# Kernel optimization log

Hardware: AMD Instinct MI355X
Metric: run time of the kernel (lower is better)

## Reference

```python
import jax, jax.numpy as jnp
import numpy as np

N, E, F_IN, HID, HEADS, NCLS, NG = 50000, 800000, 128, 128, 4, 10, 512
C = HID // HEADS          # per-head channels
BN_EPS = 1e-5
NEG_SLOPE = 0.2           # SuperGATConv default negative_slope
N_CONV = 3


def setup_inputs() -> dict:
    key = jax.random.key(0)
    ks = jax.random.split(key, 16)
    x = jax.random.normal(ks[0], (N, F_IN), jnp.float32)
    # edges with no self loops (reference appends self loops itself, as SuperGATConv does)
    src = jax.random.randint(ks[1], (E,), 0, N, dtype=jnp.int32)
    off = jax.random.randint(ks[2], (E,), 1, N, dtype=jnp.int32)
    dst = (src + off) % N
    edge_index = jnp.stack([src, dst], axis=0)
    batch = jnp.sort(jax.random.randint(ks[3], (N,), 0, NG, dtype=jnp.int32))
    s = 0.1
    # BatchNorm params per module init: weight=1, bias=1e-4 (running stats fresh: mean=0, var=1)
    inp = {
        "x": x, "edge_index": edge_index, "batch": batch,
        "bn_feat_g": jnp.ones((F_IN,), jnp.float32), "bn_feat_b": jnp.full((F_IN,), 1e-4, jnp.float32),
        "w_feat": jax.random.normal(ks[4], (F_IN, HID), jnp.float32) * s,
        "b_feat": jnp.zeros((HID,), jnp.float32),
        "bn_conv_g": jnp.ones((N_CONV, HID), jnp.float32), "bn_conv_b": jnp.full((N_CONV, HID), 1e-4, jnp.float32),
        "w_gat": jax.random.normal(ks[5], (N_CONV, HID, HID), jnp.float32) * s,
        "att_l": jax.random.normal(ks[6], (N_CONV, HEADS, C), jnp.float32) * s,
        "att_r": jax.random.normal(ks[7], (N_CONV, HEADS, C), jnp.float32) * s,
        "b_gat": jnp.zeros((N_CONV, HID), jnp.float32),
        "bn_fc_g": jnp.ones((HID,), jnp.float32), "bn_fc_b": jnp.full((HID,), 1e-4, jnp.float32),
        "w_fc": jax.random.normal(ks[8], (HID, HID), jnp.float32) * s,
        "b_fc": jnp.zeros((HID,), jnp.float32),
        "bn_hid_g": jnp.ones((HID,), jnp.float32), "bn_hid_b": jnp.full((HID,), 1e-4, jnp.float32),
        "w_cls": jax.random.normal(ks[9], (HID, NCLS), jnp.float32) * s,
        "b_cls": jnp.zeros((NCLS,), jnp.float32),
    }
    return inp


def _bn_eval(h, g, b):
    # eval-mode BatchNorm1d with fresh running stats (mean=0, var=1)
    return h * (g / jnp.sqrt(1.0 + BN_EPS)) + b


def _segment_softmax(a, seg, num_segments):
    # softmax over edges grouped by destination node (PyG softmax semantics)
    m = jax.ops.segment_max(a, seg, num_segments=num_segments)
    a = jnp.exp(a - m[seg])
    s = jax.ops.segment_sum(a, seg, num_segments=num_segments)
    return a / (s[seg] + 1e-16)


def _supergat_mx(h, src, dst, W, att_l, att_r, bias):
    # h: [N, HID] -> per-head features [N, H, C]
    hh = (h @ W).reshape(N, HEADS, C)
    h_j = hh[src]  # source (message) features  [E2, H, C]
    h_i = hh[dst]  # destination features       [E2, H, C]
    logits = jnp.einsum('ehc,ehc->eh', h_i, h_j)                       # MX dot-product
    alpha = jnp.einsum('ehc,hc->eh', h_j, att_l) + jnp.einsum('ehc,hc->eh', h_i, att_r)
    alpha = alpha * jax.nn.sigmoid(logits)
    alpha = jax.nn.leaky_relu(alpha, NEG_SLOPE)
    alpha = _segment_softmax(alpha, dst, N)                            # [E2, H]
    out = jax.ops.segment_sum(h_j * alpha[..., None], dst, num_segments=N)
    return out.reshape(N, HID) + bias


def reference(x, edge_index, batch, bn_feat_g, bn_feat_b, w_feat, b_feat,
              bn_conv_g, bn_conv_b, w_gat, att_l, att_r, b_gat,
              bn_fc_g, bn_fc_b, w_fc, b_fc, bn_hid_g, bn_hid_b, w_cls, b_cls):
    loops = jnp.arange(N, dtype=edge_index.dtype)
    src = jnp.concatenate([edge_index[0], loops])   # SuperGATConv adds self loops
    dst = jnp.concatenate([edge_index[1], loops])
    h = _bn_eval(x, bn_feat_g, bn_feat_b)
    h = jax.nn.relu(h @ w_feat + b_feat)            # GCNConv(gfn=True) == Linear
    for i in range(N_CONV):
        h = _bn_eval(h, bn_conv_g[i], bn_conv_b[i])
        h = jax.nn.relu(_supergat_mx(h, src, dst, w_gat[i], att_l[i], att_r[i], b_gat[i]))
    g = jax.ops.segment_sum(h, batch, num_segments=NG)  # global_add_pool -> [NG, HID]
    g = _bn_eval(g, bn_fc_g, bn_fc_b)
    g = jax.nn.relu(g @ w_fc + b_fc)
    g = _bn_eval(g, bn_hid_g, bn_hid_b)
    logits = g @ w_cls + b_cls
    att_loss = jnp.float32(0.0)  # eval mode: no edge-sampled attention loss
    return jax.nn.log_softmax(logits, axis=-1), att_loss
```

## Files before the change

### kernel.cpp

```cpp
#include <hip/hip_runtime.h>

#define NN 50000
#define EE 800000
#define FHID 128
#define NHEAD 4
#define NGRAPH 512
#define NCLS 10
#define BK 256
#define BCH 4096
#define NBLK_E 196
#define NBUCK 196
#define CAPB 6144

typedef unsigned short u16;
typedef unsigned int u32;
typedef unsigned long long u64;
typedef __attribute__((ext_vector_type(8))) short bf16x8;
typedef __attribute__((ext_vector_type(4))) float f32x4;

__device__ __forceinline__ float bf2f(u16 u){
    union { u32 i; float f; } v; v.i = ((u32)u) << 16; return v.f;
}
__device__ __forceinline__ float bflo(u32 u){
    union { u32 i; float f; } v; v.i = u << 16; return v.f;
}
__device__ __forceinline__ float bfhi(u32 u){
    union { u32 i; float f; } v; v.i = u & 0xffff0000u; return v.f;
}
__device__ __forceinline__ u16 f2bf(float f){
    union { float f; u32 i; } v; v.f = f;
    u32 r = v.i + 0x7fffu + ((v.i >> 16) & 1u);
    return (u16)(r >> 16);
}
__device__ __forceinline__ u32 pack2(float a, float b){
    return ((u32)f2bf(b) << 16) | f2bf(a);
}
__device__ __forceinline__ float loadF(const void* p, int i, int isf32){
    return isf32 ? ((const float*)p)[i] : bf2f(((const u16*)p)[i]);
}
__device__ __forceinline__ void unpk8(uint4 v, float* f){
    f[0]=bflo(v.x); f[1]=bfhi(v.x);
    f[2]=bflo(v.y); f[3]=bfhi(v.y);
    f[4]=bflo(v.z); f[5]=bfhi(v.z);
    f[6]=bflo(v.w); f[7]=bfhi(v.w);
}

__device__ int detect_local(const u16* x, int tid, int nthreads, int* lds){
    int ok = 0;
    for (int i = tid; i < 1024; i += nthreads){
        u16 u = x[i];
        int e = (u >> 7) & 0xFF;
        if ((u & 0x7fff) == 0 || (e >= 0x70 && e <= 0x85)) ok++;
    }
    lds[tid] = ok;
    __syncthreads();
    for (int o2 = nthreads >> 1; o2 > 0; o2 >>= 1){
        if (tid < o2) lds[tid] += lds[tid + o2];
        __syncthreads();
    }
    int r = (lds[0] < 900) ? 1 : 0;
    __syncthreads();
    return r;
}

__global__ __launch_bounds__(256) void prep_all(
        const u16* __restrict__ xz,
        const void* w_feat, const void* b_feat, const void* bn_feat_g, const void* bn_feat_b,
        const void* w_gat, const void* bn_conv_g, const void* bn_conv_b, const void* b_gat,
        const void* wfc, const void* bfc, const void* bnfg, const void* bnfb,
        const void* bnhg, const void* bnhb, const void* wcls, const void* bcls,
        const void* attl, const void* attr,
        u16* __restrict__ Wt, float* __restrict__ cvec, float* __restrict__ biasv,
        float* __restrict__ hp, int* __restrict__ dflag, int* __restrict__ gcur)
{
    __shared__ int ldsi[256];
    __shared__ float red[128];
    int bid = blockIdx.x, t = threadIdx.x;
    int isf32 = detect_local(xz, t, 256, ldsi);
    if (bid == 0){
        if (t == 0) dflag[0] = isf32;
        gcur[t] = t * CAPB;
    }

    if (bid < 512){
        if (t >= 128) return;
        int L = bid >> 7;
        int n = bid & 127;
        int k = t;
        const float rs = rsqrtf(1.0f + 1e-5f);
        float wv, bg, bb;
        if (L == 0){
            wv = loadF(w_feat, k*FHID + n, isf32);
            bg = loadF(bn_feat_g, k, isf32);
            bb = loadF(bn_feat_b, k, isf32);
        } else {
            wv = loadF(w_gat, (L-1)*FHID*FHID + k*FHID + n, isf32);
            bg = loadF(bn_conv_g, (L-1)*FHID + k, isf32);
            bb = loadF(bn_conv_b, (L-1)*FHID + k, isf32);
        }
        Wt[L*FHID*FHID + n*FHID + k] = f2bf(bg * rs * wv);
        red[k] = bb * wv;
        __syncthreads();
        for (int o2 = 64; o2 > 0; o2 >>= 1){
            if (k < o2) red[k] += red[k + o2];
            __syncthreads();
        }
        if (k == 0){
            float c = red[0];
            if (L == 0) c += loadF(b_feat, n, isf32);
            cvec[L*FHID + n] = c;
            if (L > 0) biasv[L*FHID + n] = loadF(b_gat, (L-1)*FHID + n, isf32);
        }
    } else {
        int gt = (bid - 512)*256 + t;
        for (int i = gt; i < FHID*FHID; i += 16*256) hp[i] = loadF(wfc, i, isf32);
        if (gt < FHID*NCLS) hp[16384 + gt] = loadF(wcls, gt, isf32);
        if (gt >= 2048 && gt < 2048 + 3*FHID){
            int i = gt - 2048;
            hp[18320 + i] = loadF(attl, i, isf32);
            hp[18704 + i] = loadF(attr, i, isf32);
        }
        if (gt >= 2560 && gt < 2560 + FHID){
            int tt = gt - 2560;
            hp[17664 + tt] = loadF(bnfg, tt, isf32);
            hp[17792 + tt] = loadF(bnfb, tt, isf32);
            hp[17920 + tt] = loadF(bfc,  tt, isf32);
            hp[18048 + tt] = loadF(bnhg, tt, isf32);
            hp[18176 + tt] = loadF(bnhb, tt, isf32);
        }
        if (gt >= 3072 && gt < 3072 + NCLS) hp[18304 + (gt - 3072)] = loadF(bcls, gt - 3072, isf32);
    }
}

__global__ __launch_bounds__(256) void gemm128(const void* __restrict__ A,
                                               const u16* __restrict__ Wt,
                                               const float* __restrict__ cvec,
                                               u16* __restrict__ out, int relu,
                                               int araw, const int* __restrict__ flag,
                                               const float* __restrict__ attl,
                                               const float* __restrict__ attr,
                                               float* __restrict__ al,
                                               float* __restrict__ ar)
{
    int wave = threadIdx.x >> 6;
    int lane = threadIdx.x & 63;
    int m = lane & 15, quad = lane >> 4;
    int rowbase = blockIdx.x * 128 + wave * 32;
    bool f32in = araw && flag[0];
    const u16*  Au = (const u16*)A;
    const float* Af = (const float*)A;
    int r0 = rowbase + m, r1 = rowbase + 16 + m;
    bool v0 = r0 < NN, v1 = r1 < NN;
    f32x4 acc[2][8];
#pragma unroll
    for (int i = 0; i < 2; i++)
#pragma unroll
        for (int j = 0; j < 8; j++) acc[i][j] = (f32x4){0.f,0.f,0.f,0.f};
#pragma unroll
    for (int t = 0; t < 4; t++){
        bf16x8 a0 = {0,0,0,0,0,0,0,0}, a1 = {0,0,0,0,0,0,0,0};
        int kof = t*32 + quad*8;
        if (f32in){
            if (v0){
                const float* p = Af + (size_t)r0*FHID + kof;
                float4 u0 = *(const float4*)p, u1 = *(const float4*)(p+4);
                a0[0]=(short)f2bf(u0.x); a0[1]=(short)f2bf(u0.y);
                a0[2]=(short)f2bf(u0.z); a0[3]=(short)f2bf(u0.w);
                a0[4]=(short)f2bf(u1.x); a0[5]=(short)f2bf(u1.y);
                a0[6]=(short)f2bf(u1.z); a0[7]=(short)f2bf(u1.w);
            }
            if (v1){
                const float* p = Af + (size_t)r1*FHID + kof;
                float4 u0 = *(const float4*)p, u1 = *(const float4*)(p+4);
                a1[0]=(short)f2bf(u0.x); a1[1]=(short)f2bf(u0.y);
                a1[2]=(short)f2bf(u0.z); a1[3]=(short)f2bf(u0.w);
                a1[4]=(short)f2bf(u1.x); a1[5]=(short)f2bf(u1.y);
                a1[6]=(short)f2bf(u1.z); a1[7]=(short)f2bf(u1.w);
            }
        } else {
            if (v0) a0 = *(const bf16x8*)(Au + (size_t)r0*FHID + kof);
            if (v1) a1 = *(const bf16x8*)(Au + (size_t)r1*FHID + kof);
        }
#pragma unroll
        for (int ct = 0; ct < 8; ct++){
            bf16x8 wfrag = *(const bf16x8*)(Wt + (ct*16 + m)*FHID + kof);
            acc[0][ct] = __builtin_amdgcn_mfma_f32_16x16x32_bf16(wfrag, a0, acc[0][ct], 0, 0, 0);
            acc[1][ct] = __builtin_amdgcn_mfma_f32_16x16x32_bf16(wfrag, a1, acc[1][ct], 0, 0, 0);
        }
    }
    bool doa = (attl != nullptr);
#pragma unroll
    for (int tt = 0; tt < 2; tt++){
        int row = rowbase + tt*16 + m;
        bool rv = row < NN;
        float sl[4] = {0.f,0.f,0.f,0.f};
        float sr[4] = {0.f,0.f,0.f,0.f};
#pragma unroll
        for (int ct = 0; ct < 8; ct++){
            int cb = ct*16 + quad*4;
            float4 cv = *(const float4*)(cvec + cb);
            float w0 = acc[tt][ct][0] + cv.x;
            float w1 = acc[tt][ct][1] + cv.y;
            float w2 = acc[tt][ct][2] + cv.z;
            float w3 = acc[tt][ct][3] + cv.w;
            if (relu){
                w0 = fmaxf(w0, 0.f); w1 = fmaxf(w1, 0.f);
                w2 = fmaxf(w2, 0.f); w3 = fmaxf(w3, 0.f);
            }
            if (doa){
                int h = ct >> 1;
                float4 tl = *(const float4*)(attl + cb);
                float4 tr = *(const float4*)(attr + cb);
                sl[h] += w0*tl.x + w1*tl.y + w2*tl.z + w3*tl.w;
                sr[h] += w0*tr.x + w1*tr.y + w2*tr.z + w3*tr.w;
            }
            if (rv){
                uint2 st; st.x = pack2(w0, w1); st.y = pack2(w2, w3);
                *(uint2*)(out + (size_t)row*FHID + cb) = st;
            }
        }
        if (doa){
#pragma unroll
            for (int h = 0; h < 4; h++){
                sl[h] += __shfl_xor(sl[h], 16, 64);
                sl[h] += __shfl_xor(sl[h], 32, 64);
                sr[h] += __shfl_xor(sr[h], 16, 64);
                sr[h] += __shfl_xor(sr[h], 32, 64);
            }
            if (rv){
                al[row*NHEAD + quad] = sl[quad];
                ar[row*NHEAD + quad] = sr[quad];
            }
        }
    }
}

__global__ __launch_bounds__(256) void bin_edges(const int* __restrict__ srcp,
        const int* __restrict__ dstp, int* __restrict__ gcur, u64* __restrict__ binned)
{
    __shared__ int h[BK], lb[BK], gb[BK], cur[BK];
    __shared__ u64 stage[BCH];
    int t = threadIdx.x;
    h[t] = 0;
    __syncthreads();
    int base = blockIdx.x * BCH;
    int sv[16], dv[16];
#pragma unroll
    for (int k = 0; k < 16; k++){
        int e = base + k*256 + t;
        int d = -1, s = 0;
        if (e < EE){
            d = dstp[e]; s = srcp[e];
            if ((u32)d >= NN) d = -1;
        }
        sv[k] = s; dv[k] = d;
        if (d >= 0) atomicAdd(&h[d >> 8], 1);
    }
    __syncthreads();
    lb[t] = h[t];
    __syncthreads();
    for (int off = 1; off < BK; off <<= 1){
        int x = (t >= off) ? lb[t - off] : 0;
        __syncthreads();
        lb[t] += x;
        __syncthreads();
    }
    int excl = lb[t] - h[t];
    int tot  = lb[BK-1];
    __syncthreads();
    lb[t] = excl;
    gb[t] = h[t] ? atomicAdd(&gcur[t], h[t]) : 0;
    cur[t] = 0;
    __syncthreads();
#pragma unroll
    for (int k = 0; k < 16; k++){
        int d = dv[k];
        if (d >= 0){
            int b = d >> 8;
            int p = lb[b] + atomicAdd(&cur[b], 1);
            stage[p] = ((u64)(u32)d << 32) | (u32)sv[k];
        }
    }
    __syncthreads();
    for (int i = t; i < tot; i += 256){
        u64 pr = stage[i];
        int b = (int)(pr >> 40);
        binned[gb[b] + (i - lb[b])] = pr;
    }
}

__global__ __launch_bounds__(256) void build_csr(const u64* __restrict__ binned,
        const int* __restrict__ gcur, int2* __restrict__ rowdeg, int* __restrict__ colbuf)
{
    __shared__ int deg[BK], ls[BK], cur[BK];
    __shared__ int colstage[CAPB];
    int b = blockIdx.x, t = threadIdx.x;
    int gb = b * CAPB;
    int cnt = gcur[b] - gb;
    if (cnt < 0) cnt = 0;
    if (cnt > CAPB) cnt = CAPB;
    deg[t] = 0;
    __syncthreads();
    for (int i = t; i < cnt; i += 256){
        int d = (int)(binned[gb + i] >> 32);
        atomicAdd(&deg[d & 255], 1);
    }
    __syncthreads();
    ls[t] = deg[t];
    __syncthreads();
    for (int off = 1; off < BK; off <<= 1){
        int x = (t >= off) ? ls[t - off] : 0;
        __syncthreads();
        ls[t] += x;
        __syncthreads();
    }
    int excl = ls[t] - deg[t];
    int node = b*256 + t;
    if (node < NN) rowdeg[node] = (int2){gb + excl, gb + excl + deg[t]};
    cur[t] = excl;
    __syncthreads();
    for (int i = t; i < cnt; i += 256){
        u64 pr = binned[gb + i];
        int d = (int)(pr >> 32) & 255;
        int s = (int)(u32)pr;
        int p = atomicAdd(&cur[d], 1);
        colstage[p] = s;
    }
    __syncthreads();
    for (int i = t; i < cnt; i += 256) colbuf[gb + i] = colstage[i];
}

__global__ __launch_bounds__(256) void supergat_conv(const u16* __restrict__ hh,
        const float* __restrict__ al, const float* __restrict__ ar,
        const int2* __restrict__ rowdeg, const int* __restrict__ colbuf,
        const float* __restrict__ bias, u16* __restrict__ hout)
{
    int wid  = (blockIdx.x*256 + threadIdx.x) >> 6;
    int lane = threadIdx.x & 63;
    int group = lane >> 4;
    int gl    = lane & 15;
    int head  = gl >> 2;
    int q     = gl & 3;
    int node  = wid*4 + group;
    bool valid = node < NN;
    int snode = valid ? node : 0;
    int chbase = head*32 + q*8;

    uint4 hdv = *(const uint4*)(hh + (size_t)snode*FHID + chbase);
    float hd[8]; unpk8(hdv, hd);
    float arn = ar[snode*NHEAD + head];
    float aln = al[snode*NHEAD + head];

    float d = hd[0]*hd[0]+hd[1]*hd[1]+hd[2]*hd[2]+hd[3]*hd[3]
            + hd[4]*hd[4]+hd[5]*hd[5]+hd[6]*hd[6]+hd[7]*hd[7];
    d += __shfl_xor(d, 1, 64);
    d += __shfl_xor(d, 2, 64);
    float a = (aln + arn) * (1.0f / (1.0f + __expf(-d)));
    a = (a > 0.0f) ? a : 0.2f*a;
    float p = __expf(fminf(a, 60.f));
    float s = p;
    float o[8];
#pragma unroll
    for (int i = 0; i < 8; i++) o[i] = p*hd[i];

    int2 rd = valid ? rowdeg[node] : (int2){0,0};
    int e0 = rd.x, e1 = rd.y;
    if (e0 < 0) e0 = 0;
    if (e1 > BK*CAPB) e1 = BK*CAPB;

    int e = e0;
    while (e + 3 < e1){
        int sidx[4]; uint4 xv[4]; float af[4];
#pragma unroll
        for (int j = 0; j < 4; j++){
            int si = colbuf[e + j];
            if ((u32)si >= NN) si = 0;
            sidx[j] = si;
        }
#pragma unroll
        for (int j = 0; j < 4; j++){
            xv[j] = *(const uint4*)(hh + (size_t)sidx[j]*FHID + chbase);
            af[j] = al[sidx[j]*NHEAD + head];
        }
#pragma unroll
        for (int j = 0; j < 4; j++){
            float hs[8]; unpk8(xv[j], hs);
            float lg = hd[0]*hs[0]+hd[1]*hs[1]+hd[2]*hs[2]+hd[3]*hs[3]
                     + hd[4]*hs[4]+hd[5]*hs[5]+hd[6]*hs[6]+hd[7]*hs[7];
            lg += __shfl_xor(lg, 1, 64);
            lg += __shfl_xor(lg, 2, 64);
            float a2 = (af[j] + arn) * (1.0f / (1.0f + __expf(-lg)));
            a2 = (a2 > 0.0f) ? a2 : 0.2f*a2;
            float pe = __expf(fminf(a2, 60.f));
            s += pe;
#pragma unroll
            for (int i = 0; i < 8; i++) o[i] += pe*hs[i];
        }
        e += 4;
    }
    while (e < e1){
        int si = colbuf[e];
        if ((u32)si >= NN) si = 0;
        uint4 x1 = *(const uint4*)(hh + (size_t)si*FHID + chbase);
        float af1 = al[si*NHEAD + head];
        float hs[8]; unpk8(x1, hs);
        float lg = hd[0]*hs[0]+hd[1]*hs[1]+hd[2]*hs[2]+hd[3]*hs[3]
                 + hd[4]*hs[4]+hd[5]*hs[5]+hd[6]*hs[6]+hd[7]*hs[7];
        lg += __shfl_xor(lg, 1, 64);
        lg += __shfl_xor(lg, 2, 64);
        float a2 = (af1 + arn) * (1.0f / (1.0f + __expf(-lg)));
        a2 = (a2 > 0.0f) ? a2 : 0.2f*a2;
        float pe = __expf(fminf(a2, 60.f));
        s += pe;
#pragma unroll
        for (int i = 0; i < 8; i++) o[i] += pe*hs[i];
        e++;
    }

    if (valid){
        float inv = 1.0f / (s + 1e-16f);
        uint4 w;
        w.x = pack2(fmaxf(o[0]*inv + bias[chbase+0], 0.f),
                    fmaxf(o[1]*inv + bias[chbase+1], 0.f));
        w.y = pack2(fmaxf(o[2]*inv + bias[chbase+2], 0.f),
                    fmaxf(o[3]*inv + bias[chbase+3], 0.f));
        w.z = pack2(fmaxf(o[4]*inv + bias[chbase+4], 0.f),
                    fmaxf(o[5]*inv + bias[chbase+5], 0.f));
        w.w = pack2(fmaxf(o[6]*inv + bias[chbase+6], 0.f),
                    fmaxf(o[7]*inv + bias[chbase+7], 0.f));
        *(uint4*)(hout + (size_t)node*FHID + chbase) = w;
    }
}

__global__ void pool_head(const u16* __restrict__ h, const int* __restrict__ batch,
                          const float* __restrict__ hp, const int* __restrict__ flag,
                          void* __restrict__ out)
{
    __shared__ int bounds[2];
    __shared__ float gb[FHID];
    __shared__ float g2[FHID];
    __shared__ float lg[16];
    int gi = blockIdx.x, t = threadIdx.x;
    int isf32 = flag[0];
    if (t < 2){
        int target = gi + t;
        int lo = 0, hi = NN;
        while (lo < hi){
            int mid = (lo + hi) >> 1;
            if (batch[mid] < target) lo = mid + 1; else hi = mid;
        }
        bounds[t] = lo;
    }
    __syncthreads();
    float acc0 = 0.f;
    for (int node = bounds[0]; node < bounds[1]; node++)
        acc0 += bf2f(h[(size_t)node*FHID + t]);
    const float rs = rsqrtf(1.0f + 1e-5f);
    gb[t] = acc0 * (hp[17664 + t] * rs) + hp[17792 + t];
    __syncthreads();
    float acc = hp[17920 + t];
    for (int k = 0; k < FHID; k++) acc += gb[k] * hp[k*FHID + t];
    acc = fmaxf(acc, 0.f);
    g2[t] = acc * (hp[18048 + t] * rs) + hp[18176 + t];
    __syncthreads();
    if (t < NCLS){
        float l = hp[18304 + t];
        for (int k = 0; k < FHID; k++) l += g2[k] * hp[16384 + k*NCLS + t];
        lg[t] = l;
    }
    __syncthreads();
    if (t == 0){
        float mx = lg[0];
        for (int j = 1; j < NCLS; j++) mx = fmaxf(mx, lg[j]);
        float se = 0.f;
        for (int j = 0; j < NCLS; j++) se += __expf(lg[j] - mx);
        float lse = logf(se) + mx;
        if (isf32){
            float* o = (float*)out;
            for (int j = 0; j < NCLS; j++) o[gi*NCLS + j] = lg[j] - lse;
            if (gi == 0) o[NGRAPH*NCLS] = 0.f;
        } else {
            u16* o = (u16*)out;
            for (int j = 0; j < NCLS; j++) o[gi*NCLS + j] = f2bf(lg[j] - lse);
            if (gi == 0) o[NGRAPH*NCLS] = 0;
        }
    }
}

extern "C" void kernel_launch(void* const* d_in, const int* in_sizes, int n_in,
                              void* d_out, int out_size, void* d_ws, size_t ws_size,
                              hipStream_t stream)
{
    (void)in_sizes; (void)n_in; (void)out_size; (void)ws_size;
    const void* x         = d_in[0];
    const int* edge       = (const int*)d_in[1];
    const int* batch      = (const int*)d_in[2];

    char* ws = (char*)d_ws;
    size_t off = 0;
    auto alloc = [&](size_t bytes) -> char* {
        char* p = ws + off; off += (bytes + 255) & ~(size_t)255; return p;
    };
    int*   dflag   = (int*)  alloc(256);
    u16*   WtAll   = (u16*)  alloc((size_t)4*FHID*FHID*2);
    float* cvecAll = (float*)alloc((size_t)4*FHID*4);
    float* biasv   = (float*)alloc((size_t)4*FHID*4);
    float* headp   = (float*)alloc((size_t)19088*4);
    float* al      = (float*)alloc((size_t)NN*NHEAD*4);
    float* ar      = (float*)alloc((size_t)NN*NHEAD*4);
    int*   gcur    = (int*)  alloc((size_t)BK*4);
    int2*  rowdeg  = (int2*) alloc((size_t)NN*8);
    int*   colbuf  = (int*)  alloc((size_t)BK*CAPB*4);
    u16*   hA      = (u16*)  alloc((size_t)NN*FHID*2);
    u16*   hB      = (u16*)  alloc((size_t)NN*FHID*2);
    u64*   binned  = (u64*)hB;

    const int* srcp = edge;
    const int* dstp = edge + EE;

    prep_all<<<528, 256, 0, stream>>>((const u16*)x,
        d_in[5], d_in[6], d_in[3], d_in[4], d_in[9], d_in[7], d_in[8], d_in[12],
        d_in[15], d_in[16], d_in[13], d_in[14], d_in[17], d_in[18], d_in[19], d_in[20],
        d_in[10], d_in[11],
        WtAll, cvecAll, biasv, headp, dflag, gcur);

    bin_edges<<<NBLK_E, 256, 0, stream>>>(srcp, dstp, gcur, binned);
    build_csr<<<NBUCK, 256, 0, stream>>>(binned, gcur, rowdeg, colbuf);

    gemm128<<<(NN + 127)/128, 256, 0, stream>>>(x, WtAll, cvecAll, hA, 1, 1, dflag,
                                                nullptr, nullptr, nullptr, nullptr);

    for (int i = 0; i < 3; i++){
        gemm128<<<(NN + 127)/128, 256, 0, stream>>>(hA, WtAll + (i+1)*FHID*FHID,
                                                    cvecAll + (i+1)*FHID, hB, 0, 0, dflag,
                                                    headp + 18320 + i*FHID,
                                                    headp + 18704 + i*FHID, al, ar);
        supergat_conv<<<(NN + 15)/16, 256, 0, stream>>>(hB, al, ar, rowdeg, colbuf,
                                                        biasv + (i+1)*FHID, hA);
    }

    pool_head<<<NGRAPH, 128, 0, stream>>>(hA, batch, headp, dflag, d_out);
}
```

Before: 389.7 us.

## Software-pipeline edge gathers, use DPP reductions, retile GEMM and edge binning

The supergat_conv edge loop becomes double-buffered: the next group of four neighbor rows and attention logits is loaded while the current group is computed. A masked tail replaces the scalar remainder loop, and colbuf is padded so the over-read stays in bounds. Quad reductions switch from shuffles to DPP moves. The GEMM drops to 16 rows per wave to double the grid, bin_edges uses smaller chunks across more blocks, build_csr runs with 512 threads, and pool_head unrolls its node sum into four accumulators. These changes target latency-bound gathers and low occupancy, at the cost of more weight-fragment reloads per row in the GEMM and more atomics in binning.

```diff
diff --git a/kernel.cpp b/kernel.cpp
--- a/kernel.cpp
+++ b/kernel.cpp
@@ -7,8 +7,8 @@
 #define NGRAPH 512
 #define NCLS 10
 #define BK 256
-#define BCH 4096
-#define NBLK_E 196
+#define BCH 2048
+#define NBLK_E 391
 #define NBUCK 196
 #define CAPB 6144
 
@@ -43,6 +43,13 @@
     f[2]=bflo(v.y); f[3]=bfhi(v.y);
     f[4]=bflo(v.z); f[5]=bfhi(v.z);
     f[6]=bflo(v.w); f[7]=bfhi(v.w);
+}
+
+__device__ __forceinline__ float quad_red(float x){
+    int t0 = __builtin_amdgcn_mov_dpp(__float_as_int(x), 0xB1, 0xF, 0xF, true);
+    float y = x + __int_as_float(t0);
+    int t1 = __builtin_amdgcn_mov_dpp(__float_as_int(y), 0x4E, 0xF, 0xF, true);
+    return y + __int_as_float(t1);
 }
 
 __device__ int detect_local(const u16* x, int tid, int nthreads, int* lds){
@@ -145,92 +152,74 @@
     int wave = threadIdx.x >> 6;
     int lane = threadIdx.x & 63;
     int m = lane & 15, quad = lane >> 4;
-    int rowbase = blockIdx.x * 128 + wave * 32;
+    int row = blockIdx.x * 64 + wave * 16 + m;
+    bool v0 = row < NN;
     bool f32in = araw && flag[0];
     const u16*  Au = (const u16*)A;
     const float* Af = (const float*)A;
-    int r0 = rowbase + m, r1 = rowbase + 16 + m;
-    bool v0 = r0 < NN, v1 = r1 < NN;
-    f32x4 acc[2][8];
-#pragma unroll
-    for (int i = 0; i < 2; i++)
-#pragma unroll
-        for (int j = 0; j < 8; j++) acc[i][j] = (f32x4){0.f,0.f,0.f,0.f};
+    f32x4 acc[8];
+#pragma unroll
+    for (int j = 0; j < 8; j++) acc[j] = (f32x4){0.f,0.f,0.f,0.f};
 #pragma unroll
     for (int t = 0; t < 4; t++){
-        bf16x8 a0 = {0,0,0,0,0,0,0,0}, a1 = {0,0,0,0,0,0,0,0};
+        bf16x8 a0 = {0,0,0,0,0,0,0,0};
         int kof = t*32 + quad*8;
         if (f32in){
             if (v0){
-                const float* p = Af + (size_t)r0*FHID + kof;
+                const float* p = Af + (size_t)row*FHID + kof;
                 float4 u0 = *(const float4*)p, u1 = *(const float4*)(p+4);
                 a0[0]=(short)f2bf(u0.x); a0[1]=(short)f2bf(u0.y);
                 a0[2]=(short)f2bf(u0.z); a0[3]=(short)f2bf(u0.w);
                 a0[4]=(short)f2bf(u1.x); a0[5]=(short)f2bf(u1.y);
                 a0[6]=(short)f2bf(u1.z); a0[7]=(short)f2bf(u1.w);
             }
-            if (v1){
-                const float* p = Af + (size_t)r1*FHID + kof;
-                float4 u0 = *(const float4*)p, u1 = *(const float4*)(p+4);
-                a1[0]=(short)f2bf(u0.x); a1[1]=(short)f2bf(u0.y);
-                a1[2]=(short)f2bf(u0.z); a1[3]=(short)f2bf(u0.w);
-                a1[4]=(short)f2bf(u1.x); a1[5]=(short)f2bf(u1.y);
-                a1[6]=(short)f2bf(u1.z); a1[7]=(short)f2bf(u1.w);
-            }
         } else {
-            if (v0) a0 = *(const bf16x8*)(Au + (size_t)r0*FHID + kof);
-            if (v1) a1 = *(const bf16x8*)(Au + (size_t)r1*FHID + kof);
+            if (v0) a0 = *(const bf16x8*)(Au + (size_t)row*FHID + kof);
         }
 #pragma unroll
         for (int ct = 0; ct < 8; ct++){
             bf16x8 wfrag = *(const bf16x8*)(Wt + (ct*16 + m)*FHID + kof);
-            acc[0][ct] = __builtin_amdgcn_mfma_f32_16x16x32_bf16(wfrag, a0, acc[0][ct], 0, 0, 0);
-            acc[1][ct] = __builtin_amdgcn_mfma_f32_16x16x32_bf16(wfrag, a1, acc[1][ct], 0, 0, 0);
+            acc[ct] = __builtin_amdgcn_mfma_f32_16x16x32_bf16(wfrag, a0, acc[ct], 0, 0, 0);
         }
     }
     bool doa = (attl != nullptr);
-#pragma unroll
-    for (int tt = 0; tt < 2; tt++){
-        int row = rowbase + tt*16 + m;
-        bool rv = row < NN;
-        float sl[4] = {0.f,0.f,0.f,0.f};
-        float sr[4] = {0.f,0.f,0.f,0.f};
-#pragma unroll
-        for (int ct = 0; ct < 8; ct++){
-            int cb = ct*16 + quad*4;
-            float4 cv = *(const float4*)(cvec + cb);
-            float w0 = acc[tt][ct][0] + cv.x;
-            float w1 = acc[tt][ct][1] + cv.y;
-            float w2 = acc[tt][ct][2] + cv.z;
-            float w3 = acc[tt][ct][3] + cv.w;
-            if (relu){
-                w0 = fmaxf(w0, 0.f); w1 = fmaxf(w1, 0.f);
-                w2 = fmaxf(w2, 0.f); w3 = fmaxf(w3, 0.f);
-            }
-            if (doa){
-                int h = ct >> 1;
-                float4 tl = *(const float4*)(attl + cb);
-                float4 tr = *(const float4*)(attr + cb);
-                sl[h] += w0*tl.x + w1*tl.y + w2*tl.z + w3*tl.w;
-                sr[h] += w0*tr.x + w1*tr.y + w2*tr.z + w3*tr.w;
-            }
-            if (rv){
-                uint2 st; st.x = pack2(w0, w1); st.y = pack2(w2, w3);
-                *(uint2*)(out + (size_t)row*FHID + cb) = st;
-            }
+    float sl[4] = {0.f,0.f,0.f,0.f};
+    float sr[4] = {0.f,0.f,0.f,0.f};
+#pragma unroll
+    for (int ct = 0; ct < 8; ct++){
+        int cb = ct*16 + quad*4;
+        float4 cv = *(const float4*)(cvec + cb);
+        float w0 = acc[ct][0] + cv.x;
+        float w1 = acc[ct][1] + cv.y;
+        float w2 = acc[ct][2] + cv.z;
+        float w3 = acc[ct][3] + cv.w;
+        if (relu){
+            w0 = fmaxf(w0, 0.f); w1 = fmaxf(w1, 0.f);
+            w2 = fmaxf(w2, 0.f); w3 = fmaxf(w3, 0.f);
         }
         if (doa){
-#pragma unroll
-            for (int h = 0; h < 4; h++){
-                sl[h] += __shfl_xor(sl[h], 16, 64);
-                sl[h] += __shfl_xor(sl[h], 32, 64);
-                sr[h] += __shfl_xor(sr[h], 16, 64);
-                sr[h] += __shfl_xor(sr[h], 32, 64);
-            }
-            if (rv){
-                al[row*NHEAD + quad] = sl[quad];
-                ar[row*NHEAD + quad] = sr[quad];
-            }
+            int h = ct >> 1;
+            float4 tl = *(const float4*)(attl + cb);
+            float4 tr = *(const float4*)(attr + cb);
+            sl[h] += w0*tl.x + w1*tl.y + w2*tl.z + w3*tl.w;
+            sr[h] += w0*tr.x + w1*tr.y + w2*tr.z + w3*tr.w;
+        }
+        if (v0){
+            uint2 st; st.x = pack2(w0, w1); st.y = pack2(w2, w3);
+            *(uint2*)(out + (size_t)row*FHID + cb) = st;
+        }
+    }
+    if (doa){
+#pragma unroll
+        for (int h = 0; h < 4; h++){
+            sl[h] += __shfl_xor(sl[h], 16, 64);
+            sl[h] += __shfl_xor(sl[h], 32, 64);
+            sr[h] += __shfl_xor(sr[h], 16, 64);
+            sr[h] += __shfl_xor(sr[h], 32, 64);
+        }
+        if (v0){
+            al[row*NHEAD + quad] = sl[quad];
+            ar[row*NHEAD + quad] = sr[quad];
         }
     }
 }
@@ -244,9 +233,9 @@
     h[t] = 0;
     __syncthreads();
     int base = blockIdx.x * BCH;
-    int sv[16], dv[16];
-#pragma unroll
-    for (int k = 0; k < 16; k++){
+    int sv[8], dv[8];
+#pragma unroll
+    for (int k = 0; k < 8; k++){
         int e = base + k*256 + t;
         int d = -1, s = 0;
         if (e < EE){
@@ -273,7 +262,7 @@
     cur[t] = 0;
     __syncthreads();
 #pragma unroll
-    for (int k = 0; k < 16; k++){
+    for (int k = 0; k < 8; k++){
         int d = dv[k];
         if (d >= 0){
             int b = d >> 8;
@@ -289,7 +278,7 @@
     }
 }
 
-__global__ __launch_bounds__(256) void build_csr(const u64* __restrict__ binned,
+__global__ __launch_bounds__(512) void build_csr(const u64* __restrict__ binned,
         const int* __restrict__ gcur, int2* __restrict__ rowdeg, int* __restrict__ colbuf)
 {
     __shared__ int deg[BK], ls[BK], cur[BK];
@@ -299,27 +288,29 @@
     int cnt = gcur[b] - gb;
     if (cnt < 0) cnt = 0;
     if (cnt > CAPB) cnt = CAPB;
-    deg[t] = 0;
-    __syncthreads();
-    for (int i = t; i < cnt; i += 256){
+    if (t < BK) deg[t] = 0;
+    __syncthreads();
+    for (int i = t; i < cnt; i += 512){
         int d = (int)(binned[gb + i] >> 32);
         atomicAdd(&deg[d & 255], 1);
     }
     __syncthreads();
-    ls[t] = deg[t];
+    if (t < BK) ls[t] = deg[t];
     __syncthreads();
     for (int off = 1; off < BK; off <<= 1){
-        int x = (t >= off) ? ls[t - off] : 0;
+        int x = (t < BK && t >= off) ? ls[t - off] : 0;
         __syncthreads();
-        ls[t] += x;
+        if (t < BK) ls[t] += x;
         __syncthreads();
     }
-    int excl = ls[t] - deg[t];
-    int node = b*256 + t;
-    if (node < NN) rowdeg[node] = (int2){gb + excl, gb + excl + deg[t]};
-    cur[t] = excl;
-    __syncthreads();
-    for (int i = t; i < cnt; i += 256){
+    if (t < BK){
+        int excl = ls[t] - deg[t];
+        int node = b*256 + t;
+        if (node < NN) rowdeg[node] = (int2){gb + excl, gb + excl + deg[t]};
+        cur[t] = excl;
+    }
+    __syncthreads();
+    for (int i = t; i < cnt; i += 512){
         u64 pr = binned[gb + i];
         int d = (int)(pr >> 32) & 255;
         int s = (int)(u32)pr;
@@ -327,7 +318,56 @@
         colstage[p] = s;
     }
     __syncthreads();
-    for (int i = t; i < cnt; i += 256) colbuf[gb + i] = colstage[i];
+    for (int i = t; i < cnt; i += 512) colbuf[gb + i] = colstage[i];
+}
+
+struct EdgeGrp {
+    uint4 x0, x1, x2, x3;
+    float f0, f1, f2, f3;
+};
+
+__device__ __forceinline__ void load_grp(EdgeGrp& G, const int* __restrict__ colbuf,
+        int g, const u16* __restrict__ hh, const float* __restrict__ al,
+        int chbase, int head)
+{
+    int i0 = colbuf[g+0], i1 = colbuf[g+1], i2 = colbuf[g+2], i3 = colbuf[g+3];
+    if ((u32)i0 >= NN) i0 = 0;
+    if ((u32)i1 >= NN) i1 = 0;
+    if ((u32)i2 >= NN) i2 = 0;
+    if ((u32)i3 >= NN) i3 = 0;
+    G.x0 = *(const uint4*)(hh + (size_t)i0*FHID + chbase);
+    G.x1 = *(const uint4*)(hh + (size_t)i1*FHID + chbase);
+    G.x2 = *(const uint4*)(hh + (size_t)i2*FHID + chbase);
+    G.x3 = *(const uint4*)(hh + (size_t)i3*FHID + chbase);
+    G.f0 = al[i0*NHEAD + head];
+    G.f1 = al[i1*NHEAD + head];
+    G.f2 = al[i2*NHEAD + head];
+    G.f3 = al[i3*NHEAD + head];
+}
+
+__device__ __forceinline__ void comp_edge(uint4 xv, float af, bool ev,
+        const float* hd, float arn, float& s, float* o)
+{
+    float hs[8]; unpk8(xv, hs);
+    float lg = hd[0]*hs[0]+hd[1]*hs[1]+hd[2]*hs[2]+hd[3]*hs[3]
+             + hd[4]*hs[4]+hd[5]*hs[5]+hd[6]*hs[6]+hd[7]*hs[7];
+    lg = quad_red(lg);
+    float a2 = (af + arn) * (1.0f / (1.0f + __expf(-lg)));
+    a2 = (a2 > 0.0f) ? a2 : 0.2f*a2;
+    float pe = __expf(fminf(a2, 60.f));
+    if (!ev) pe = 0.f;
+    s += pe;
+#pragma unroll
+    for (int i = 0; i < 8; i++) o[i] += pe*hs[i];
+}
+
+__device__ __forceinline__ void comp_grp(const EdgeGrp& G, int g, int e1,
+        const float* hd, float arn, float& s, float* o)
+{
+    comp_edge(G.x0, G.f0, g+0 < e1, hd, arn, s, o);
+    comp_edge(G.x1, G.f1, g+1 < e1, hd, arn, s, o);
+    comp_edge(G.x2, G.f2, g+2 < e1, hd, arn, s, o);
+    comp_edge(G.x3, G.f3, g+3 < e1, hd, arn, s, o);
 }
 
 __global__ __launch_bounds__(256) void supergat_conv(const u16* __restrict__ hh,
@@ -353,8 +393,7 @@
 
     float d = hd[0]*hd[0]+hd[1]*hd[1]+hd[2]*hd[2]+hd[3]*hd[3]
             + hd[4]*hd[4]+hd[5]*hd[5]+hd[6]*hd[6]+hd[7]*hd[7];
-    d += __shfl_xor(d, 1, 64);
-    d += __shfl_xor(d, 2, 64);
+    d = quad_red(d);
     float a = (aln + arn) * (1.0f / (1.0f + __expf(-d)));
     a = (a > 0.0f) ? a : 0.2f*a;
     float p = __expf(fminf(a, 60.f));
@@ -368,53 +407,21 @@
     if (e0 < 0) e0 = 0;
     if (e1 > BK*CAPB) e1 = BK*CAPB;
 
-    int e = e0;
-    while (e + 3 < e1){
-        int sidx[4]; uint4 xv[4]; float af[4];
-#pragma unroll
-        for (int j = 0; j < 4; j++){
-            int si = colbuf[e + j];
-            if ((u32)si >= NN) si = 0;
-            sidx[j] = si;
-        }
-#pragma unroll
-        for (int j = 0; j < 4; j++){
-            xv[j] = *(const uint4*)(hh + (size_t)sidx[j]*FHID + chbase);
-            af[j] = al[sidx[j]*NHEAD + head];
-        }
-#pragma unroll
-        for (int j = 0; j < 4; j++){
-            float hs[8]; unpk8(xv[j], hs);
-            float lg = hd[0]*hs[0]+hd[1]*hs[1]+hd[2]*hs[2]+hd[3]*hs[3]
-                     + hd[4]*hs[4]+hd[5]*hs[5]+hd[6]*hs[6]+hd[7]*hs[7];
-            lg += __shfl_xor(lg, 1, 64);
-            lg += __shfl_xor(lg, 2, 64);
-            float a2 = (af[j] + arn) * (1.0f / (1.0f + __expf(-lg)));
-            a2 = (a2 > 0.0f) ? a2 : 0.2f*a2;
-            float pe = __expf(fminf(a2, 60.f));
-            s += pe;
-#pragma unroll
-            for (int i = 0; i < 8; i++) o[i] += pe*hs[i];
-        }
-        e += 4;
-    }
-    while (e < e1){
-        int si = colbuf[e];
-        if ((u32)si >= NN) si = 0;
-        uint4 x1 = *(const uint4*)(hh + (size_t)si*FHID + chbase);
-        float af1 = al[si*NHEAD + head];
-        float hs[8]; unpk8(x1, hs);
-        float lg = hd[0]*hs[0]+hd[1]*hs[1]+hd[2]*hs[2]+hd[3]*hs[3]
-                 + hd[4]*hs[4]+hd[5]*hs[5]+hd[6]*hs[6]+hd[7]*hs[7];
-        lg += __shfl_xor(lg, 1, 64);
-        lg += __shfl_xor(lg, 2, 64);
-        float a2 = (af1 + arn) * (1.0f / (1.0f + __expf(-lg)));
-        a2 = (a2 > 0.0f) ? a2 : 0.2f*a2;
-        float pe = __expf(fminf(a2, 60.f));
-        s += pe;
-#pragma unroll
-        for (int i = 0; i < 8; i++) o[i] += pe*hs[i];
-        e++;
+    EdgeGrp A, B;
+    int g = e0;
+    if (g < e1){
+        load_grp(A, colbuf, g, hh, al, chbase, head);
+        while (true){
+            int gn = g + 4;
+            if (gn >= e1){ comp_grp(A, g, e1, hd, arn, s, o); break; }
+            load_grp(B, colbuf, gn, hh, al, chbase, head);
+            comp_grp(A, g, e1, hd, arn, s, o);
+            g = gn; gn = g + 4;
+            if (gn >= e1){ comp_grp(B, g, e1, hd, arn, s, o); break; }
+            load_grp(A, colbuf, gn, hh, al, chbase, head);
+            comp_grp(B, g, e1, hd, arn, s, o);
+            g = gn;
+        }
     }
 
     if (valid){
@@ -452,9 +459,16 @@
         bounds[t] = lo;
     }
     __syncthreads();
-    float acc0 = 0.f;
-    for (int node = bounds[0]; node < bounds[1]; node++)
-        acc0 += bf2f(h[(size_t)node*FHID + t]);
+    float s0 = 0.f, s1 = 0.f, s2 = 0.f, s3 = 0.f;
+    int node = bounds[0], nend = bounds[1];
+    for (; node + 3 < nend; node += 4){
+        s0 += bf2f(h[(size_t)(node+0)*FHID + t]);
+        s1 += bf2f(h[(size_t)(node+1)*FHID + t]);
+        s2 += bf2f(h[(size_t)(node+2)*FHID + t]);
+        s3 += bf2f(h[(size_t)(node+3)*FHID + t]);
+    }
+    for (; node < nend; node++) s0 += bf2f(h[(size_t)node*FHID + t]);
+    float acc0 = (s0 + s1) + (s2 + s3);
     const float rs = rsqrtf(1.0f + 1e-5f);
     gb[t] = acc0 * (hp[17664 + t] * rs) + hp[17792 + t];
     __syncthreads();
@@ -510,7 +524,7 @@
     float* ar      = (float*)alloc((size_t)NN*NHEAD*4);
     int*   gcur    = (int*)  alloc((size_t)BK*4);
     int2*  rowdeg  = (int2*) alloc((size_t)NN*8);
-    int*   colbuf  = (int*)  alloc((size_t)BK*CAPB*4);
+    int*   colbuf  = (int*)  alloc((size_t)(BK*CAPB + 16)*4);
     u16*   hA      = (u16*)  alloc((size_t)NN*FHID*2);
     u16*   hB      = (u16*)  alloc((size_t)NN*FHID*2);
     u64*   binned  = (u64*)hB;
@@ -525,16 +539,16 @@
         WtAll, cvecAll, biasv, headp, dflag, gcur);
 
     bin_edges<<<NBLK_E, 256, 0, stream>>>(srcp, dstp, gcur, binned);
-    build_csr<<<NBUCK, 256, 0, stream>>>(binned, gcur, rowdeg, colbuf);
-
-    gemm128<<<(NN + 127)/128, 256, 0, stream>>>(x, WtAll, cvecAll, hA, 1, 1, dflag,
-                                                nullptr, nullptr, nullptr, nullptr);
+    build_csr<<<NBUCK, 512, 0, stream>>>(binned, gcur, rowdeg, colbuf);
+
+    gemm128<<<(NN + 63)/64, 256, 0, stream>>>(x, WtAll, cvecAll, hA, 1, 1, dflag,
+                                              nullptr, nullptr, nullptr, nullptr);
 
     for (int i = 0; i < 3; i++){
-        gemm128<<<(NN + 127)/128, 256, 0, stream>>>(hA, WtAll + (i+1)*FHID*FHID,
-                                                    cvecAll + (i+1)*FHID, hB, 0, 0, dflag,
-                                                    headp + 18320 + i*FHID,
-                                                    headp + 18704 + i*FHID, al, ar);
+        gemm128<<<(NN + 63)/64, 256, 0, stream>>>(hA, WtAll + (i+1)*FHID*FHID,
+                                                  cvecAll + (i+1)*FHID, hB, 0, 0, dflag,
+                                                  headp + 18320 + i*FHID,
+                                                  headp + 18704 + i*FHID, al, ar);
         supergat_conv<<<(NN + 15)/16, 256, 0, stream>>>(hB, al, ar, rowdeg, colbuf,
                                                         biasv + (i+1)*FHID, hA);
     }
```

After: 414.0 us. 1.06x slower.
